# Kernel optimization log

Hardware: AMD Instinct MI355X
Metric: run time of the kernel (lower is better)

The kernel has to match this reference:

```python
import jax, jax.numpy as jnp
import numpy as np

GROUP_SIZE = 128

def _dequantize(qweight, wscales, wzeros):
    # qweight: [N, K//2] packed bytes, two uint4 values per byte
    # low nibble = even k index, high nibble = odd k index
    N, Kh = qweight.shape
    K = Kh * 2
    low = qweight & 0xF
    high = (qweight >> 4) & 0xF
    w_int = jnp.stack([low, high], axis=-1).reshape(N, K).astype(jnp.float32)  # [N, K]
    G = K // GROUP_SIZE  # number of groups along K
    w_grp = w_int.reshape(N, G, GROUP_SIZE)
    s = wscales.T.reshape(N, G, 1)   # wscales: [G, N] -> [N, G, 1]
    z = wzeros.T.reshape(N, G, 1)
    return ((w_grp - z) * s).reshape(N, K)  # [N, K] dequantized

def setup_inputs() -> dict:
    key = jax.random.key(0)
    k1, k2, k3, k4, k5 = jax.random.split(key, 5)
    M, K, N = 4096, 4096, 12288
    G = K // GROUP_SIZE
    x = jax.random.normal(k1, (M, K), dtype=jnp.float32)
    qweight = jax.random.randint(k2, (N, K // 2), 0, 256, dtype=jnp.int32)
    wscales = jax.random.uniform(k3, (G, N), dtype=jnp.float32) * 0.05
    wzeros = jax.random.uniform(k4, (G, N), dtype=jnp.float32) * 15.0
    bias = jax.random.normal(k5, (N,), dtype=jnp.float32)
    return {"x": x, "qweight": qweight, "wscales": wscales, "wzeros": wzeros, "bias": bias}

def reference(x, qweight, wscales, wzeros, bias):
    # AWQ W4A16 linear: y = x @ dequant(W)^T + b
    w = _dequantize(qweight, wscales, wzeros)  # [N, K]
    return jnp.einsum('mk,nk->mn', x, w) + bias
```

## Files before the change

kernel.cpp:

```cpp
#include <hip/hip_runtime.h>

#define M_DIM 4096
#define K_DIM 4096
#define N_DIM 12288
#define BM 256
#define BN 256
#define BK 64
#define NT (K_DIM / BK)

typedef __bf16 bf16x8  __attribute__((ext_vector_type(8)));
typedef float  floatx16 __attribute__((ext_vector_type(16)));

__global__ __launch_bounds__(256) void xcast_kernel(const float* __restrict__ x,
                                                    __bf16* __restrict__ xb) {
    int idx = blockIdx.x * 256 + threadIdx.x;
    const float4* xv = (const float4*)x;
    float4 a = xv[idx * 2];
    float4 b = xv[idx * 2 + 1];
    bf16x8 o;
    o[0] = (__bf16)a.x; o[1] = (__bf16)a.y; o[2] = (__bf16)a.z; o[3] = (__bf16)a.w;
    o[4] = (__bf16)b.x; o[5] = (__bf16)b.y; o[6] = (__bf16)b.z; o[7] = (__bf16)b.w;
    ((bf16x8*)xb)[idx] = o;
}

__global__ __launch_bounds__(256) void dequant_kernel(const int* __restrict__ qw,
                                                      const float* __restrict__ scales,
                                                      const float* __restrict__ zeros,
                                                      __bf16* __restrict__ wb) {
    int idx = blockIdx.x * 256 + threadIdx.x;
    int n  = idx >> 9;
    int jq = (idx & 511) << 2;
    int g  = jq >> 6;
    float s = scales[g * N_DIM + n];
    float z = zeros[g * N_DIM + n];
    int4 q = *(const int4*)(qw + (size_t)n * (K_DIM / 2) + jq);
    bf16x8 o;
    o[0] = (__bf16)(((float)(q.x & 15)        - z) * s);
    o[1] = (__bf16)(((float)((q.x >> 4) & 15) - z) * s);
    o[2] = (__bf16)(((float)(q.y & 15)        - z) * s);
    o[3] = (__bf16)(((float)((q.y >> 4) & 15) - z) * s);
    o[4] = (__bf16)(((float)(q.z & 15)        - z) * s);
    o[5] = (__bf16)(((float)((q.z >> 4) & 15) - z) * s);
    o[6] = (__bf16)(((float)(q.w & 15)        - z) * s);
    o[7] = (__bf16)(((float)((q.w >> 4) & 15) - z) * s);
    *(bf16x8*)(wb + (size_t)n * K_DIM + (size_t)jq * 2) = o;
}

__global__ __launch_bounds__(512, 2) void gemm_kernel(const __bf16* __restrict__ A,
                                                      const __bf16* __restrict__ B,
                                                      const float* __restrict__ bias,
                                                      float* __restrict__ C) {
    __shared__ __bf16 As[2][BM * BK];
    __shared__ __bf16 Bs[2][BN * BK];

    const int tid  = threadIdx.x;
    const int wave = tid >> 6;
    const int lane = tid & 63;
    const int l32  = lane & 31;
    const int half = lane >> 5;
    const int side = wave >> 2;
    const int aw   = wave & 3;
    const int wm   = side * 128;
    const int wn   = aw * 64;
    const int bm0  = blockIdx.x * BM;
    const int bn0  = blockIdx.y * BN;

    const int rowInChunk = lane >> 3;
    const int slot       = lane & 7;
    const int gread      = (l32 & 7) ^ (((l32 >> 3) & 3) << 1);

    const int ca0 = side * 16 + aw * 2;
    const int ca1 = side * 16 + 8 + aw * 2;
    const int cb  = aw * 8 + side * 4;

    #define SRCKEY(c) (slot ^ rowInChunk ^ (((c) & 3) << 1))
    const __bf16* sA0 = A + (size_t)(bm0 + (ca0    ) * 8 + rowInChunk) * K_DIM + SRCKEY(ca0    ) * 8;
    const __bf16* sA1 = A + (size_t)(bm0 + (ca0 + 1) * 8 + rowInChunk) * K_DIM + SRCKEY(ca0 + 1) * 8;
    const __bf16* sA2 = A + (size_t)(bm0 + (ca1    ) * 8 + rowInChunk) * K_DIM + SRCKEY(ca1    ) * 8;
    const __bf16* sA3 = A + (size_t)(bm0 + (ca1 + 1) * 8 + rowInChunk) * K_DIM + SRCKEY(ca1 + 1) * 8;
    const __bf16* sB0 = B + (size_t)(bn0 + (cb     ) * 8 + rowInChunk) * K_DIM + SRCKEY(cb     ) * 8;
    const __bf16* sB1 = B + (size_t)(bn0 + (cb  + 1) * 8 + rowInChunk) * K_DIM + SRCKEY(cb  + 1) * 8;
    const __bf16* sB2 = B + (size_t)(bn0 + (cb  + 2) * 8 + rowInChunk) * K_DIM + SRCKEY(cb  + 2) * 8;
    const __bf16* sB3 = B + (size_t)(bn0 + (cb  + 3) * 8 + rowInChunk) * K_DIM + SRCKEY(cb  + 3) * 8;

    const int dA0 = (ca0    ) * 512, dA1 = (ca0 + 1) * 512;
    const int dA2 = (ca1    ) * 512, dA3 = (ca1 + 1) * 512;
    const int dB0 = (cb     ) * 512, dB1 = (cb  + 1) * 512;
    const int dB2 = (cb  + 2) * 512, dB3 = (cb  + 3) * 512;

    #define GLOAD(G, L) __builtin_amdgcn_global_load_lds( \
        (const __attribute__((address_space(1))) void*)(G), \
        (__attribute__((address_space(3))) void*)(L), 16, 0, 0)

    const int rA0 = (wm +  0 + l32) * BK;
    const int rA1 = (wm + 32 + l32) * BK;
    const int rA2 = (wm + 64 + l32) * BK;
    const int rA3 = (wm + 96 + l32) * BK;
    const int rB0 = (wn +  0 + l32) * BK;
    const int rB1 = (wn + 32 + l32) * BK;
    const int ko0 = ((0 * 2 + half) ^ gread) << 3;
    const int ko1 = ((1 * 2 + half) ^ gread) << 3;
    const int ko2 = ((2 * 2 + half) ^ gread) << 3;
    const int ko3 = ((3 * 2 + half) ^ gread) << 3;

    #define RD(P, R, KO) (*(const bf16x8*)((P) + (R) + (KO)))
    #define MF(AF, BF, ACC) __builtin_amdgcn_mfma_f32_32x32x16_bf16((AF), (BF), (ACC), 0, 0, 0)

    floatx16 acc00 = {}, acc01 = {}, acc10 = {}, acc11 = {};
    floatx16 acc20 = {}, acc21 = {}, acc30 = {}, acc31 = {};

    GLOAD(sA0, &As[0][dA0]); GLOAD(sA1, &As[0][dA1]);
    GLOAD(sB0, &Bs[0][dB0]); GLOAD(sB1, &Bs[0][dB1]);
    GLOAD(sB2, &Bs[0][dB2]); GLOAD(sB3, &Bs[0][dB3]);
    GLOAD(sA2, &As[0][dA2]); GLOAD(sA3, &As[0][dA3]);
    asm volatile("s_waitcnt vmcnt(2)" ::: "memory");
    __builtin_amdgcn_s_barrier();

    for (int kt = 0; kt < NT; ++kt) {
        const int cur = kt & 1;
        const int nxt = cur ^ 1;
        const int k0n = ((kt + 1) & (NT - 1)) * BK;
        const __bf16* Ac = &As[cur][0];
        const __bf16* Bc = &Bs[cur][0];

        GLOAD(sA0 + k0n, &As[nxt][dA0]);
        GLOAD(sA1 + k0n, &As[nxt][dA1]);
        bf16x8 a0_0 = RD(Ac, rA0, ko0), a0_1 = RD(Ac, rA0, ko1), a0_2 = RD(Ac, rA0, ko2), a0_3 = RD(Ac, rA0, ko3);
        bf16x8 a1_0 = RD(Ac, rA1, ko0), a1_1 = RD(Ac, rA1, ko1), a1_2 = RD(Ac, rA1, ko2), a1_3 = RD(Ac, rA1, ko3);
        bf16x8 b0_0 = RD(Bc, rB0, ko0), b0_1 = RD(Bc, rB0, ko1), b0_2 = RD(Bc, rB0, ko2), b0_3 = RD(Bc, rB0, ko3);
        __builtin_amdgcn_s_barrier();
        __builtin_amdgcn_s_setprio(1);
        acc00 = MF(a0_0, b0_0, acc00); acc10 = MF(a1_0, b0_0, acc10);
        acc00 = MF(a0_1, b0_1, acc00); acc10 = MF(a1_1, b0_1, acc10);
        acc00 = MF(a0_2, b0_2, acc00); acc10 = MF(a1_2, b0_2, acc10);
        acc00 = MF(a0_3, b0_3, acc00); acc10 = MF(a1_3, b0_3, acc10);
        __builtin_amdgcn_s_setprio(0);
        __builtin_amdgcn_s_barrier();

        GLOAD(sB0 + k0n, &Bs[nxt][dB0]);
        GLOAD(sB1 + k0n, &Bs[nxt][dB1]);
        bf16x8 b1_0 = RD(Bc, rB1, ko0), b1_1 = RD(Bc, rB1, ko1), b1_2 = RD(Bc, rB1, ko2), b1_3 = RD(Bc, rB1, ko3);
        __builtin_amdgcn_s_barrier();
        __builtin_amdgcn_s_setprio(1);
        acc01 = MF(a0_0, b1_0, acc01); acc11 = MF(a1_0, b1_0, acc11);
        acc01 = MF(a0_1, b1_1, acc01); acc11 = MF(a1_1, b1_1, acc11);
        acc01 = MF(a0_2, b1_2, acc01); acc11 = MF(a1_2, b1_2, acc11);
        acc01 = MF(a0_3, b1_3, acc01); acc11 = MF(a1_3, b1_3, acc11);
        __builtin_amdgcn_s_setprio(0);
        asm volatile("s_waitcnt vmcnt(4)" ::: "memory");
        __builtin_amdgcn_s_barrier();

        GLOAD(sB2 + k0n, &Bs[nxt][dB2]);
        GLOAD(sB3 + k0n, &Bs[nxt][dB3]);
        bf16x8 a2_0 = RD(Ac, rA2, ko0), a2_1 = RD(Ac, rA2, ko1), a2_2 = RD(Ac, rA2, ko2), a2_3 = RD(Ac, rA2, ko3);
        bf16x8 a3_0 = RD(Ac, rA3, ko0), a3_1 = RD(Ac, rA3, ko1), a3_2 = RD(Ac, rA3, ko2), a3_3 = RD(Ac, rA3, ko3);
        __builtin_amdgcn_s_barrier();
        __builtin_amdgcn_s_setprio(1);
        acc21 = MF(a2_0, b1_0, acc21); acc31 = MF(a3_0, b1_0, acc31);
        acc21 = MF(a2_1, b1_1, acc21); acc31 = MF(a3_1, b1_1, acc31);
        acc21 = MF(a2_2, b1_2, acc21); acc31 = MF(a3_2, b1_2, acc31);
        acc21 = MF(a2_3, b1_3, acc21); acc31 = MF(a3_3, b1_3, acc31);
        __builtin_amdgcn_s_setprio(0);
        __builtin_amdgcn_s_barrier();

        GLOAD(sA2 + k0n, &As[nxt][dA2]);
        GLOAD(sA3 + k0n, &As[nxt][dA3]);
        __builtin_amdgcn_s_setprio(1);
        acc20 = MF(a2_0, b0_0, acc20); acc30 = MF(a3_0, b0_0, acc30);
        acc20 = MF(a2_1, b0_1, acc20); acc30 = MF(a3_1, b0_1, acc30);
        acc20 = MF(a2_2, b0_2, acc20); acc30 = MF(a3_2, b0_2, acc30);
        acc20 = MF(a2_3, b0_3, acc20); acc30 = MF(a3_3, b0_3, acc30);
        __builtin_amdgcn_s_setprio(0);
        asm volatile("s_waitcnt vmcnt(2)" ::: "memory");
        __builtin_amdgcn_s_barrier();
    }

    #define EPI(ACC, MI, NI) { \
        const int col = bn0 + wn + (NI) * 32 + l32; \
        const float bv = bias[col]; \
        _Pragma("unroll") \
        for (int r = 0; r < 16; ++r) { \
            const int row = bm0 + wm + (MI) * 32 + half * 4 + (r & 3) + 8 * (r >> 2); \
            C[(size_t)row * N_DIM + col] = ACC[r] + bv; \
        } }
    EPI(acc00, 0, 0); EPI(acc01, 0, 1);
    EPI(acc10, 1, 0); EPI(acc11, 1, 1);
    EPI(acc20, 2, 0); EPI(acc21, 2, 1);
    EPI(acc30, 3, 0); EPI(acc31, 3, 1);
}

extern "C" void kernel_launch(void* const* d_in, const int* in_sizes, int n_in,
                              void* d_out, int out_size, void* d_ws, size_t ws_size,
                              hipStream_t stream) {
    const float* x      = (const float*)d_in[0];
    const int*   qw     = (const int*)d_in[1];
    const float* scales = (const float*)d_in[2];
    const float* zeros  = (const float*)d_in[3];
    const float* bias   = (const float*)d_in[4];
    float* out = (float*)d_out;

    __bf16* xb = (__bf16*)d_ws;
    __bf16* wb = (__bf16*)((char*)d_ws + (size_t)M_DIM * K_DIM * 2);

    xcast_kernel<<<(M_DIM * K_DIM / 8) / 256, 256, 0, stream>>>(x, xb);
    dequant_kernel<<<(N_DIM * (K_DIM / 2) / 4) / 256, 256, 0, stream>>>(qw, scales, zeros, wb);

    dim3 grid(M_DIM / BM, N_DIM / BN);
    gemm_kernel<<<grid, 512, 0, stream>>>(xb, wb, bias, out);
}
```

Measured before the change: 780.1 us.

## Split LDS tiles into two K-halves with new swizzle and interleaved schedule

Reorganizes the shared-memory tiles into two 32-wide K halves per buffer, each row 32 elements, with a new XOR swizzle and per-wave contiguous global-to-LDS load mapping. The main loop now runs four phases per K tile, each reading one k16 slice for all A/B fragments and issuing all eight MFMAs, with next-tile loads issued in two halves. This is meant to reduce register pressure from holding all fragments at once, improve LDS bank behavior and balance load issue across the loop. It risks more barriers per iteration and a changed ordering of the vmcnt waits.

```diff
diff --git a/kernel.cpp b/kernel.cpp
--- a/kernel.cpp
+++ b/kernel.cpp
@@ -50,8 +50,8 @@
                                                       const __bf16* __restrict__ B,
                                                       const float* __restrict__ bias,
                                                       float* __restrict__ C) {
-    __shared__ __bf16 As[2][BM * BK];
-    __shared__ __bf16 Bs[2][BN * BK];
+    __shared__ __bf16 As[2 * 2 * 256 * 32];
+    __shared__ __bf16 Bs[2 * 2 * 256 * 32];
 
     const int tid  = threadIdx.x;
     const int wave = tid >> 6;
@@ -65,113 +65,92 @@
     const int bm0  = blockIdx.x * BM;
     const int bn0  = blockIdx.y * BN;
 
-    const int rowInChunk = lane >> 3;
-    const int slot       = lane & 7;
-    const int gread      = (l32 & 7) ^ (((l32 >> 3) & 3) << 1);
-
-    const int ca0 = side * 16 + aw * 2;
-    const int ca1 = side * 16 + 8 + aw * 2;
-    const int cb  = aw * 8 + side * 4;
-
-    #define SRCKEY(c) (slot ^ rowInChunk ^ (((c) & 3) << 1))
-    const __bf16* sA0 = A + (size_t)(bm0 + (ca0    ) * 8 + rowInChunk) * K_DIM + SRCKEY(ca0    ) * 8;
-    const __bf16* sA1 = A + (size_t)(bm0 + (ca0 + 1) * 8 + rowInChunk) * K_DIM + SRCKEY(ca0 + 1) * 8;
-    const __bf16* sA2 = A + (size_t)(bm0 + (ca1    ) * 8 + rowInChunk) * K_DIM + SRCKEY(ca1    ) * 8;
-    const __bf16* sA3 = A + (size_t)(bm0 + (ca1 + 1) * 8 + rowInChunk) * K_DIM + SRCKEY(ca1 + 1) * 8;
-    const __bf16* sB0 = B + (size_t)(bn0 + (cb     ) * 8 + rowInChunk) * K_DIM + SRCKEY(cb     ) * 8;
-    const __bf16* sB1 = B + (size_t)(bn0 + (cb  + 1) * 8 + rowInChunk) * K_DIM + SRCKEY(cb  + 1) * 8;
-    const __bf16* sB2 = B + (size_t)(bn0 + (cb  + 2) * 8 + rowInChunk) * K_DIM + SRCKEY(cb  + 2) * 8;
-    const __bf16* sB3 = B + (size_t)(bn0 + (cb  + 3) * 8 + rowInChunk) * K_DIM + SRCKEY(cb  + 3) * 8;
-
-    const int dA0 = (ca0    ) * 512, dA1 = (ca0 + 1) * 512;
-    const int dA2 = (ca1    ) * 512, dA3 = (ca1 + 1) * 512;
-    const int dB0 = (cb     ) * 512, dB1 = (cb  + 1) * 512;
-    const int dB2 = (cb  + 2) * 512, dB3 = (cb  + 3) * 512;
+    const int r16  = lane >> 2;
+    const int sl4  = lane & 3;
+    const int bswz = ((lane >> 3) & 3) ^ ((lane >> 5) & 3);
+    const int key0 = sl4 ^ bswz;
+    const int key1 = key0 ^ 2;
+    const __bf16* sA0 = A + (size_t)(bm0 + 32 * wave +      r16) * K_DIM + key0 * 8;
+    const __bf16* sA1 = A + (size_t)(bm0 + 32 * wave + 16 + r16) * K_DIM + key1 * 8;
+    const __bf16* sB0 = B + (size_t)(bn0 + 32 * wave +      r16) * K_DIM + key0 * 8;
+    const __bf16* sB1 = B + (size_t)(bn0 + 32 * wave + 16 + r16) * K_DIM + key1 * 8;
+    const int dst0 = wave * 1024;
+    const int dst1 = wave * 1024 + 512;
 
     #define GLOAD(G, L) __builtin_amdgcn_global_load_lds( \
         (const __attribute__((address_space(1))) void*)(G), \
         (__attribute__((address_space(3))) void*)(L), 16, 0, 0)
 
-    const int rA0 = (wm +  0 + l32) * BK;
-    const int rA1 = (wm + 32 + l32) * BK;
-    const int rA2 = (wm + 64 + l32) * BK;
-    const int rA3 = (wm + 96 + l32) * BK;
-    const int rB0 = (wn +  0 + l32) * BK;
-    const int rB1 = (wn + 32 + l32) * BK;
-    const int ko0 = ((0 * 2 + half) ^ gread) << 3;
-    const int ko1 = ((1 * 2 + half) ^ gread) << 3;
-    const int ko2 = ((2 * 2 + half) ^ gread) << 3;
-    const int ko3 = ((3 * 2 + half) ^ gread) << 3;
+    const int swzr = ((l32 >> 1) ^ (l32 >> 3)) & 3;
+    const int koE  = ((half)     ^ swzr) << 3;
+    const int koO  = ((2 | half) ^ swzr) << 3;
+    const int rA0 = (wm +  0 + l32) * 32;
+    const int rA1 = (wm + 32 + l32) * 32;
+    const int rA2 = (wm + 64 + l32) * 32;
+    const int rA3 = (wm + 96 + l32) * 32;
+    const int rB0 = (wn +  0 + l32) * 32;
+    const int rB1 = (wn + 32 + l32) * 32;
 
-    #define RD(P, R, KO) (*(const bf16x8*)((P) + (R) + (KO)))
     #define MF(AF, BF, ACC) __builtin_amdgcn_mfma_f32_32x32x16_bf16((AF), (BF), (ACC), 0, 0, 0)
 
     floatx16 acc00 = {}, acc01 = {}, acc10 = {}, acc11 = {};
     floatx16 acc20 = {}, acc21 = {}, acc30 = {}, acc31 = {};
 
-    GLOAD(sA0, &As[0][dA0]); GLOAD(sA1, &As[0][dA1]);
-    GLOAD(sB0, &Bs[0][dB0]); GLOAD(sB1, &Bs[0][dB1]);
-    GLOAD(sB2, &Bs[0][dB2]); GLOAD(sB3, &Bs[0][dB3]);
-    GLOAD(sA2, &As[0][dA2]); GLOAD(sA3, &As[0][dA3]);
-    asm volatile("s_waitcnt vmcnt(2)" ::: "memory");
+    GLOAD(sA0,      As + dst0);        GLOAD(sA1,      As + dst1);
+    GLOAD(sB0,      Bs + dst0);        GLOAD(sB1,      Bs + dst1);
+    GLOAD(sA0 + 32, As + 8192 + dst0); GLOAD(sA1 + 32, As + 8192 + dst1);
+    GLOAD(sB0 + 32, Bs + 8192 + dst0); GLOAD(sB1 + 32, Bs + 8192 + dst1);
+    asm volatile("s_waitcnt vmcnt(4)" ::: "memory");
     __builtin_amdgcn_s_barrier();
 
+    #define READS(HOFF, KO) \
+        a0 = *(const bf16x8*)(As + curo + (HOFF) + rA0 + (KO)); \
+        b0 = *(const bf16x8*)(Bs + curo + (HOFF) + rB0 + (KO)); \
+        a1 = *(const bf16x8*)(As + curo + (HOFF) + rA1 + (KO)); \
+        b1 = *(const bf16x8*)(Bs + curo + (HOFF) + rB1 + (KO)); \
+        a2 = *(const bf16x8*)(As + curo + (HOFF) + rA2 + (KO)); \
+        a3 = *(const bf16x8*)(As + curo + (HOFF) + rA3 + (KO));
+
+    #define MFMAS \
+        __builtin_amdgcn_s_setprio(1); \
+        acc00 = MF(a0, b0, acc00); acc10 = MF(a1, b0, acc10); \
+        acc01 = MF(a0, b1, acc01); acc11 = MF(a1, b1, acc11); \
+        acc20 = MF(a2, b0, acc20); acc21 = MF(a2, b1, acc21); \
+        acc30 = MF(a3, b0, acc30); acc31 = MF(a3, b1, acc31); \
+        __builtin_amdgcn_s_setprio(0);
+
     for (int kt = 0; kt < NT; ++kt) {
-        const int cur = kt & 1;
-        const int nxt = cur ^ 1;
-        const int k0n = ((kt + 1) & (NT - 1)) * BK;
-        const __bf16* Ac = &As[cur][0];
-        const __bf16* Bc = &Bs[cur][0];
+        const int curo = (kt & 1) * 16384;
+        const int nxto = 16384 - curo;
+        const int k0n  = ((kt + 1) & (NT - 1)) * BK;
+        bf16x8 a0, a1, a2, a3, b0, b1;
 
-        GLOAD(sA0 + k0n, &As[nxt][dA0]);
-        GLOAD(sA1 + k0n, &As[nxt][dA1]);
-        bf16x8 a0_0 = RD(Ac, rA0, ko0), a0_1 = RD(Ac, rA0, ko1), a0_2 = RD(Ac, rA0, ko2), a0_3 = RD(Ac, rA0, ko3);
-        bf16x8 a1_0 = RD(Ac, rA1, ko0), a1_1 = RD(Ac, rA1, ko1), a1_2 = RD(Ac, rA1, ko2), a1_3 = RD(Ac, rA1, ko3);
-        bf16x8 b0_0 = RD(Bc, rB0, ko0), b0_1 = RD(Bc, rB0, ko1), b0_2 = RD(Bc, rB0, ko2), b0_3 = RD(Bc, rB0, ko3);
+        READS(0, koE);
         __builtin_amdgcn_s_barrier();
-        __builtin_amdgcn_s_setprio(1);
-        acc00 = MF(a0_0, b0_0, acc00); acc10 = MF(a1_0, b0_0, acc10);
-        acc00 = MF(a0_1, b0_1, acc00); acc10 = MF(a1_1, b0_1, acc10);
-        acc00 = MF(a0_2, b0_2, acc00); acc10 = MF(a1_2, b0_2, acc10);
-        acc00 = MF(a0_3, b0_3, acc00); acc10 = MF(a1_3, b0_3, acc10);
-        __builtin_amdgcn_s_setprio(0);
+        MFMAS;
         __builtin_amdgcn_s_barrier();
 
-        GLOAD(sB0 + k0n, &Bs[nxt][dB0]);
-        GLOAD(sB1 + k0n, &Bs[nxt][dB1]);
-        bf16x8 b1_0 = RD(Bc, rB1, ko0), b1_1 = RD(Bc, rB1, ko1), b1_2 = RD(Bc, rB1, ko2), b1_3 = RD(Bc, rB1, ko3);
-        __builtin_amdgcn_s_barrier();
-        __builtin_amdgcn_s_setprio(1);
-        acc01 = MF(a0_0, b1_0, acc01); acc11 = MF(a1_0, b1_0, acc11);
-        acc01 = MF(a0_1, b1_1, acc01); acc11 = MF(a1_1, b1_1, acc11);
-        acc01 = MF(a0_2, b1_2, acc01); acc11 = MF(a1_2, b1_2, acc11);
-        acc01 = MF(a0_3, b1_3, acc01); acc11 = MF(a1_3, b1_3, acc11);
-        __builtin_amdgcn_s_setprio(0);
+        READS(0, koO);
+        GLOAD(sA0 + k0n, As + nxto + dst0); GLOAD(sA1 + k0n, As + nxto + dst1);
+        GLOAD(sB0 + k0n, Bs + nxto + dst0); GLOAD(sB1 + k0n, Bs + nxto + dst1);
         asm volatile("s_waitcnt vmcnt(4)" ::: "memory");
         __builtin_amdgcn_s_barrier();
-
-        GLOAD(sB2 + k0n, &Bs[nxt][dB2]);
-        GLOAD(sB3 + k0n, &Bs[nxt][dB3]);
-        bf16x8 a2_0 = RD(Ac, rA2, ko0), a2_1 = RD(Ac, rA2, ko1), a2_2 = RD(Ac, rA2, ko2), a2_3 = RD(Ac, rA2, ko3);
-        bf16x8 a3_0 = RD(Ac, rA3, ko0), a3_1 = RD(Ac, rA3, ko1), a3_2 = RD(Ac, rA3, ko2), a3_3 = RD(Ac, rA3, ko3);
-        __builtin_amdgcn_s_barrier();
-        __builtin_amdgcn_s_setprio(1);
-        acc21 = MF(a2_0, b1_0, acc21); acc31 = MF(a3_0, b1_0, acc31);
-        acc21 = MF(a2_1, b1_1, acc21); acc31 = MF(a3_1, b1_1, acc31);
-        acc21 = MF(a2_2, b1_2, acc21); acc31 = MF(a3_2, b1_2, acc31);
-        acc21 = MF(a2_3, b1_3, acc21); acc31 = MF(a3_3, b1_3, acc31);
-        __builtin_amdgcn_s_setprio(0);
+        MFMAS;
         __builtin_amdgcn_s_barrier();
 
-        GLOAD(sA2 + k0n, &As[nxt][dA2]);
-        GLOAD(sA3 + k0n, &As[nxt][dA3]);
-        __builtin_amdgcn_s_setprio(1);
-        acc20 = MF(a2_0, b0_0, acc20); acc30 = MF(a3_0, b0_0, acc30);
-        acc20 = MF(a2_1, b0_1, acc20); acc30 = MF(a3_1, b0_1, acc30);
-        acc20 = MF(a2_2, b0_2, acc20); acc30 = MF(a3_2, b0_2, acc30);
-        acc20 = MF(a2_3, b0_3, acc20); acc30 = MF(a3_3, b0_3, acc30);
-        __builtin_amdgcn_s_setprio(0);
-        asm volatile("s_waitcnt vmcnt(2)" ::: "memory");
+        READS(8192, koE);
+        __builtin_amdgcn_s_barrier();
+        MFMAS;
+        __builtin_amdgcn_s_barrier();
+
+        READS(8192, koO);
+        GLOAD(sA0 + k0n + 32, As + nxto + 8192 + dst0);
+        GLOAD(sA1 + k0n + 32, As + nxto + 8192 + dst1);
+        GLOAD(sB0 + k0n + 32, Bs + nxto + 8192 + dst0);
+        GLOAD(sB1 + k0n + 32, Bs + nxto + 8192 + dst1);
+        asm volatile("s_waitcnt vmcnt(4)" ::: "memory");
+        __builtin_amdgcn_s_barrier();
+        MFMAS;
         __builtin_amdgcn_s_barrier();
     }
 
```

Result: faster. 729.1 us (-6.5%).
